# Performance work log

Measured on AMD Instinct MI355X. Metric: run time of the kernel, lower is better.

Reference implementation:

```python
import jax, jax.numpy as jnp
import numpy as np

TAU = 3.0
K = 3
EPS = 1e-8


def _normalize(x):
    # L2-normalize over last dim with clamped norm (matches torch clamp(min=eps))
    n = jnp.clip(jnp.linalg.norm(x, axis=-1, keepdims=True), EPS, None)
    return x / n


def get_sim(im, s):
    # im: [N, R, D], s: [P, L, D] -> sim [N, P]
    im_n = _normalize(im)
    s_n = _normalize(s)
    scores = jnp.einsum('nrd,pld->nprl', im_n, s_n)  # cosine per (region, token)
    return scores.max(axis=2).sum(axis=2)            # max over regions, sum over tokens


def semantic_transfer_loss(m1_n, m1_p, m2_p):
    sim = get_sim(m1_n, m1_p)                        # [Bn, Bp]
    m1_k, idx = jax.lax.top_k(sim, K)                # [Bn, K]
    m2_k_emb = m2_p[idx]                             # [Bn, K, L2, D]
    im_n = _normalize(m1_n)
    s_n = _normalize(m2_k_emb)
    scores = jnp.einsum('nrd,nkld->nkrl', im_n, s_n) # [Bn, K, R, L2]
    m2_k = scores.max(axis=2).sum(axis=2)            # [Bn, K]
    log_q = jax.nn.log_softmax(m2_k / TAU, axis=-1)
    log_p = jax.nn.log_softmax(m1_k / TAU, axis=-1)
    p = jnp.exp(log_p)
    # F.kl_div(log_q, p, reduction='sum') = sum p * (log p - log q)
    return jnp.sum(p * (log_p - log_q))


def setup_inputs() -> dict:
    key = jax.random.key(0)
    k1, k2, k3, k4 = jax.random.split(key, 4)
    B, R, L, D = 256, 36, 32, 1024
    return {
        'img_n_emb': jax.random.normal(k1, (B, R, D), dtype=jnp.float32),
        'cap_n_emb': jax.random.normal(k2, (B, L, D), dtype=jnp.float32),
        'img_p_emb': jax.random.normal(k3, (B, R, D), dtype=jnp.float32),
        'cap_p_emb': jax.random.normal(k4, (B, L, D), dtype=jnp.float32),
    }


def reference(img_n_emb, cap_n_emb, img_p_emb, cap_p_emb):
    loss = (semantic_transfer_loss(img_n_emb, img_p_emb, cap_p_emb)
            + semantic_transfer_loss(cap_n_emb, cap_p_emb, img_p_emb))
    return loss
```

## Files before the change

### kernel.cpp

```cpp
#include <hip/hip_runtime.h>
#include <math.h>

#define TAU 3.0f
#define NB 256
#define DD 1024
#define KSEL 3

typedef _Float16 half8 __attribute__((ext_vector_type(8)));
typedef _Float16 half4 __attribute__((ext_vector_type(4)));
typedef float f32x4 __attribute__((ext_vector_type(4)));

__device__ __forceinline__ void gload_lds16(const void* g, void* l) {
    __builtin_amdgcn_global_load_lds(
        (const __attribute__((address_space(1))) unsigned int*)g,
        (__attribute__((address_space(3))) unsigned int*)l, 16, 0, 0);
}

__device__ __forceinline__ unsigned int fenc(float x) {
    unsigned int u = __float_as_uint(x);
    return u ^ (((unsigned int)((int)u >> 31)) | 0x80000000u);
}
__device__ __forceinline__ float fdec(unsigned int e) {
    unsigned int u = (e & 0x80000000u) ? (e ^ 0x80000000u) : ~e;
    return __uint_as_float(u);
}

__global__ __launch_bounds__(256) void norm_split_kernel(
    const float* __restrict__ x, _Float16* __restrict__ hi, _Float16* __restrict__ lo,
    float* __restrict__ inv)
{
    int row = blockIdx.x;
    int tid = threadIdx.x;
    const float* p = x + (size_t)row * DD;
    float4 v = reinterpret_cast<const float4*>(p)[tid];
    float ss = fmaf(v.x, v.x, fmaf(v.y, v.y, fmaf(v.z, v.z, v.w * v.w)));
#pragma unroll
    for (int off = 32; off; off >>= 1) ss += __shfl_down(ss, off);
    __shared__ float red[4];
    if ((tid & 63) == 0) red[tid >> 6] = ss;
    __syncthreads();
    float tot = red[0] + red[1] + red[2] + red[3];
    float nrm = fmaxf(sqrtf(tot), 1e-8f);
    if (tid == 0) inv[row] = 1.0f / nrm;
    float xn[4] = { v.x / nrm, v.y / nrm, v.z / nrm, v.w / nrm };
    half4 h, l;
#pragma unroll
    for (int i = 0; i < 4; ++i) {
        _Float16 hh = (_Float16)xn[i];
        h[i] = hh;
        l[i] = (_Float16)(xn[i] - (float)hh);
    }
    *reinterpret_cast<half4*>(hi + (size_t)row * DD + tid * 4) = h;
    *reinterpret_cast<half4*>(lo + (size_t)row * DD + tid * 4) = l;
}

template<int G, int THREADS>
__global__ __launch_bounds__(THREADS, 1) void mfma_simX_kernel(
    const _Float16* __restrict__ Ah, const _Float16* __restrict__ Al,
    const _Float16* __restrict__ Bh, const _Float16* __restrict__ Bl,
    unsigned int* __restrict__ cmax, int Wc)
{
    constexpr int TM = 192, TN = 192, WGM = 2, WGN = 3, WAVES = 6;
    static_assert(THREADS == WAVES * 64, "");
    constexpr int WMS = TM / WGM;
    constexpr int WNS = TN / WGN;
    constexpr int MF = WMS / 16;
    constexpr int NF = WNS / 16;
    constexpr int KCH = 32, NCH = DD / KCH;
    constexpr int ABYT = 2 * TM * 64;
    constexpr int BBYT = 2 * TN * 64;
    constexpr int BUFB = ABYT + BBYT;
    constexpr int NREG = BUFB / 1024;
    constexpr int RPW = NREG / WAVES;

    __shared__ __align__(16) char LDSB[2 * BUFB];

    const int bm = blockIdx.y, bn = blockIdx.x;
    const int tid = threadIdx.x;
    const int lane = tid & 63, wv = tid >> 6;
    const int wm = wv / WGN, wn = wv % WGN;
    const int col = lane & 15, grp = lane >> 4;

    const _Float16* srcp[RPW];
    int ldsoff[RPW];
    const int swz = ((lane & 3) ^ ((lane >> 3) & 3)) << 3;
#pragma unroll
    for (int i = 0; i < RPW; ++i) {
        int r = wv + i * WAVES;
        int arr = r / 12;
        int rip = (r % 12) * 16 + (lane >> 2);
        int grow = (arr < 2 ? bm * TM : bn * TN) + rip;
        const _Float16* base = (arr == 0) ? Ah : (arr == 1) ? Al : (arr == 2) ? Bh : Bl;
        srcp[i] = base + (((size_t)grow) << 10) + swz;
        ldsoff[i] = r * 1024;
    }

    f32x4 acc[MF][NF];
#pragma unroll
    for (int i = 0; i < MF; ++i)
#pragma unroll
        for (int j = 0; j < NF; ++j) acc[i][j] = (f32x4)0.f;

#pragma unroll
    for (int i = 0; i < RPW; ++i) gload_lds16(srcp[i], LDSB + ldsoff[i]);
    __syncthreads();

    for (int c = 0; c < NCH; ++c) {
        const int cb = c & 1;
        if (c + 1 < NCH) {
            const int nbuf = cb ^ 1;
#pragma unroll
            for (int i = 0; i < RPW; ++i)
                gload_lds16(srcp[i] + (c + 1) * KCH, LDSB + nbuf * BUFB + ldsoff[i]);
        }
        const char* LA  = LDSB + cb * BUFB;
        const char* LAl = LA + TM * 64;
        const char* LB  = LA + ABYT;
        const char* LBl = LB + TN * 64;

        half8 bh[NF], bl_[NF];
#pragma unroll
        for (int fn = 0; fn < NF; ++fn) {
            int row = wn * WNS + fn * 16 + col;
            int j = (grp ^ ((row >> 1) & 3)) << 4;
            bh[fn]  = *(const half8*)(LB  + row * 64 + j);
            bl_[fn] = *(const half8*)(LBl + row * 64 + j);
        }
#pragma unroll
        for (int fm = 0; fm < MF; ++fm) {
            int row = wm * WMS + fm * 16 + col;
            int j = (grp ^ ((row >> 1) & 3)) << 4;
            half8 ah  = *(const half8*)(LA  + row * 64 + j);
            half8 al_ = *(const half8*)(LAl + row * 64 + j);
#pragma unroll
            for (int fn = 0; fn < NF; ++fn) {
                acc[fm][fn] = __builtin_amdgcn_mfma_f32_16x16x32_f16(ah,  bh[fn],  acc[fm][fn], 0, 0, 0);
                acc[fm][fn] = __builtin_amdgcn_mfma_f32_16x16x32_f16(ah,  bl_[fn], acc[fm][fn], 0, 0, 0);
                acc[fm][fn] = __builtin_amdgcn_mfma_f32_16x16x32_f16(al_, bh[fn],  acc[fm][fn], 0, 0, 0);
            }
        }
        __syncthreads();
    }

    float* cm = (float*)LDSB;
    constexpr int CMS = TN + 1;
#pragma unroll
    for (int fm = 0; fm < MF; ++fm) {
        int rc = ((wm * WMS + fm * 16) >> 2) + grp;
#pragma unroll
        for (int fn = 0; fn < NF; ++fn) {
            f32x4 v = acc[fm][fn];
            float m = fmaxf(fmaxf(v[0], v[1]), fmaxf(v[2], v[3]));
            cm[rc * CMS + wn * WNS + fn * 16 + col] = m;
        }
    }
    __syncthreads();
    const int mrow0 = bm * TM;
    const int g0 = mrow0 / G;
    const int g1 = (mrow0 + TM - 1) / G;
    const int ngs = g1 - g0 + 1;
    for (int it = tid; it < ngs * TN; it += THREADS) {
        int gi = it / TN, cc = it - gi * TN;
        int g = g0 + gi;
        int rs = g * G;        if (rs < mrow0) rs = mrow0;
        int re = (g + 1) * G;  if (re > mrow0 + TM) re = mrow0 + TM;
        float m = -INFINITY;
        int rc0 = (rs - mrow0) >> 2, rc1 = (re - mrow0) >> 2;
        for (int rc = rc0; rc < rc1; ++rc) m = fmaxf(m, cm[rc * CMS + cc]);
        atomicMax(&cmax[(size_t)g * Wc + bn * TN + cc], fenc(m));
    }
}

template<int G2>
__global__ void finish_kernel(const unsigned int* __restrict__ cmax, int Wc,
                              float* __restrict__ sim) {
    int n = blockIdx.x, p = threadIdx.x;
    const unsigned int* row = cmax + (size_t)n * Wc + p * G2;
    float s = 0.f;
#pragma unroll
    for (int l = 0; l < G2; ++l) s += fdec(row[l]);
    sim[(size_t)n * NB + p] = s;
}

template<int R, int L>
__global__ __launch_bounds__(256) void blocksim_kernel(
    const float* __restrict__ A, const float* __restrict__ invA,
    const float* __restrict__ Bm, const float* __restrict__ invB,
    const int* __restrict__ bsel, int P, float* __restrict__ out)
{
    constexpr int CH = 64, CHP = 68;
    constexpr int TI = (R + 15) / 16, TJ = (L + 15) / 16;
    __shared__ __align__(16) float As[R][CHP];
    __shared__ __align__(16) float Bs[L][CHP];
    __shared__ float colmax[L];

    int t = blockIdx.x;
    int n = t / P;
    int pk = t - n * P;
    int brow = bsel ? bsel[t] : pk;

    const float* Ab = A + (size_t)n * R * DD;
    const float* Bb = Bm + (size_t)brow * L * DD;

    int tid = threadIdx.x;
    int tx = tid & 15, ty = tid >> 4;

    int ra[TI], lb[TJ];
#pragma unroll
    for (int i = 0; i < TI; ++i) ra[i] = min(ty + 16 * i, R - 1);
#pragma unroll
    for (int j = 0; j < TJ; ++j) lb[j] = min(tx + 16 * j, L - 1);

    float acc[TI][TJ];
#pragma unroll
    for (int i = 0; i < TI; ++i)
#pragma unroll
        for (int j = 0; j < TJ; ++j) acc[i][j] = 0.f;

    for (int c = 0; c < DD / CH; ++c) {
        int d0 = c * CH;
        for (int idx = tid; idx < R * CH; idx += 256) {
            int r = idx >> 6, dd = idx & 63;
            As[r][dd] = Ab[(size_t)r * DD + d0 + dd];
        }
        for (int idx = tid; idx < L * CH; idx += 256) {
            int r = idx >> 6, dd = idx & 63;
            Bs[r][dd] = Bb[(size_t)r * DD + d0 + dd];
        }
        __syncthreads();
#pragma unroll
        for (int dd = 0; dd < CH; dd += 4) {
            float4 av[TI], bv[TJ];
#pragma unroll
            for (int i = 0; i < TI; ++i) av[i] = *reinterpret_cast<const float4*>(&As[ra[i]][dd]);
#pragma unroll
            for (int j = 0; j < TJ; ++j) bv[j] = *reinterpret_cast<const float4*>(&Bs[lb[j]][dd]);
#pragma unroll
            for (int i = 0; i < TI; ++i)
#pragma unroll
                for (int j = 0; j < TJ; ++j) {
                    acc[i][j] = fmaf(av[i].x, bv[j].x, acc[i][j]);
                    acc[i][j] = fmaf(av[i].y, bv[j].y, acc[i][j]);
                    acc[i][j] = fmaf(av[i].z, bv[j].z, acc[i][j]);
                    acc[i][j] = fmaf(av[i].w, bv[j].w, acc[i][j]);
                }
        }
        __syncthreads();
    }

    float* cosS = &As[0][0];
    constexpr int LS = L + 1;
    float ia[TI];
#pragma unroll
    for (int i = 0; i < TI; ++i) ia[i] = invA[n * R + ra[i]];
#pragma unroll
    for (int j = 0; j < TJ; ++j) {
        float ib = invB[brow * L + lb[j]];
#pragma unroll
        for (int i = 0; i < TI; ++i) {
            int r = ty + 16 * i, l = tx + 16 * j;
            if (r < R && l < L) cosS[r * LS + l] = acc[i][j] * ia[i] * ib;
        }
    }
    __syncthreads();
    if (tid < L) {
        float m = -INFINITY;
        for (int r = 0; r < R; ++r) m = fmaxf(m, cosS[r * LS + tid]);
        colmax[tid] = m;
    }
    __syncthreads();
    if (tid == 0) {
        float s = 0.f;
        for (int l = 0; l < L; ++l) s += colmax[l];
        out[t] = s;
    }
}

__global__ void topk_kernel(const float* __restrict__ sim, float* __restrict__ vals,
                            int* __restrict__ outidx) {
    int n = blockIdx.x;
    int lane = threadIdx.x;
    float v0 = -INFINITY, v1 = -INFINITY, v2 = -INFINITY;
    int i0 = 0x7fffffff, i1 = 0x7fffffff, i2 = 0x7fffffff;
    for (int p = lane; p < NB; p += 64) {
        float v = sim[(size_t)n * NB + p];
        if (v > v0)      { v2 = v1; i2 = i1; v1 = v0; i1 = i0; v0 = v; i0 = p; }
        else if (v > v1) { v2 = v1; i2 = i1; v1 = v;  i1 = p; }
        else if (v > v2) { v2 = v;  i2 = p; }
    }
#pragma unroll
    for (int off = 32; off; off >>= 1) {
        float w0 = __shfl_down(v0, off), w1 = __shfl_down(v1, off), w2 = __shfl_down(v2, off);
        int   j0 = __shfl_down(i0, off), j1 = __shfl_down(i1, off), j2 = __shfl_down(i2, off);
#define INS3(w, j)                                                                   \
        if (w > v0 || (w == v0 && j < i0)) { v2=v1;i2=i1; v1=v0;i1=i0; v0=w;i0=j; }  \
        else if (w > v1 || (w == v1 && j < i1)) { v2=v1;i2=i1; v1=w;i1=j; }          \
        else if (w > v2 || (w == v2 && j < i2)) { v2=w;i2=j; }
        INS3(w0, j0); INS3(w1, j1); INS3(w2, j2);
#undef INS3
    }
    if (lane == 0) {
        vals[n * 3 + 0] = v0; vals[n * 3 + 1] = v1; vals[n * 3 + 2] = v2;
        outidx[n * 3 + 0] = i0; outidx[n * 3 + 1] = i1; outidx[n * 3 + 2] = i2;
    }
}

__global__ void loss_kernel(const float* __restrict__ m1k, const float* __restrict__ m2k,
                            float* __restrict__ out) {
    int n = threadIdx.x;
    float a[3], b[3];
#pragma unroll
    for (int i = 0; i < 3; ++i) {
        a[i] = m1k[n * 3 + i] * (1.0f / TAU);
        b[i] = m2k[n * 3 + i] * (1.0f / TAU);
    }
    float am = fmaxf(a[0], fmaxf(a[1], a[2]));
    float bm = fmaxf(b[0], fmaxf(b[1], b[2]));
    float ase = expf(a[0] - am) + expf(a[1] - am) + expf(a[2] - am);
    float bse = expf(b[0] - bm) + expf(b[1] - bm) + expf(b[2] - bm);
    float alse = am + logf(ase);
    float blse = bm + logf(bse);
    float acc = 0.f;
#pragma unroll
    for (int i = 0; i < 3; ++i) {
        float lp = a[i] - alse, lq = b[i] - blse;
        acc += expf(lp) * (lp - lq);
    }
#pragma unroll
    for (int off = 32; off; off >>= 1) acc += __shfl_down(acc, off);
    __shared__ float w[4];
    if ((threadIdx.x & 63) == 0) w[threadIdx.x >> 6] = acc;
    __syncthreads();
    if (threadIdx.x == 0) atomicAdd(out, w[0] + w[1] + w[2] + w[3]);
}

extern "C" void kernel_launch(void* const* d_in, const int* in_sizes, int n_in,
                              void* d_out, int out_size, void* d_ws, size_t ws_size,
                              hipStream_t stream) {
    const float* img_n = (const float*)d_in[0];
    const float* cap_n = (const float*)d_in[1];
    const float* img_p = (const float*)d_in[2];
    const float* cap_p = (const float*)d_in[3];
    float* out = (float*)d_out;

    char* w = (char*)d_ws;
    auto alloc = [&](size_t bytes) -> char* {
        char* p = w;
        w += (bytes + 255) & ~(size_t)255;
        return p;
    };
    const size_t IMGE  = (size_t)NB * 36 * DD;
    const size_t CAPE  = (size_t)NB * 32 * DD;
    const size_t CAPEP = (size_t)8256 * DD;

    _Float16* imgN_h = (_Float16*)alloc(IMGE * 2);
    _Float16* imgN_l = (_Float16*)alloc(IMGE * 2);
    _Float16* imgP_h = (_Float16*)alloc(IMGE * 2);
    _Float16* imgP_l = (_Float16*)alloc(IMGE * 2);
    _Float16* capN_h = (_Float16*)alloc(CAPEP * 2);
    _Float16* capN_l = (_Float16*)alloc(CAPEP * 2);
    _Float16* capP_h = (_Float16*)alloc(CAPEP * 2);
    _Float16* capP_l = (_Float16*)alloc(CAPEP * 2);

    const size_t CM1 = (size_t)256 * 9216 * 4;
    const size_t CM2 = (size_t)258 * 8256 * 4;
    unsigned int* cmaxbuf = (unsigned int*)alloc(CM1 > CM2 ? CM1 : CM2);

    float* inv_im_n  = (float*)alloc(NB * 36 * 4);
    float* inv_cap_n = (float*)alloc(NB * 32 * 4);
    float* inv_im_p  = (float*)alloc(NB * 36 * 4);
    float* inv_cap_p = (float*)alloc(NB * 32 * 4);
    float* sim1 = (float*)alloc(NB * NB * 4);
    float* sim2 = (float*)alloc(NB * NB * 4);
    float* m1k1 = (float*)alloc(NB * 3 * 4);
    float* m2k1 = (float*)alloc(NB * 3 * 4);
    float* m1k2 = (float*)alloc(NB * 3 * 4);
    float* m2k2 = (float*)alloc(NB * 3 * 4);
    int* idx1 = (int*)alloc(NB * 3 * 4);
    int* idx2 = (int*)alloc(NB * 3 * 4);

    hipMemsetAsync(d_out, 0, sizeof(float), stream);
    hipMemsetAsync(cmaxbuf, 0, CM1, stream);
    hipMemsetAsync(capN_h + CAPE, 0, (CAPEP - CAPE) * 2, stream);
    hipMemsetAsync(capN_l + CAPE, 0, (CAPEP - CAPE) * 2, stream);
    hipMemsetAsync(capP_h + CAPE, 0, (CAPEP - CAPE) * 2, stream);
    hipMemsetAsync(capP_l + CAPE, 0, (CAPEP - CAPE) * 2, stream);

    norm_split_kernel<<<NB * 36, 256, 0, stream>>>(img_n, imgN_h, imgN_l, inv_im_n);
    norm_split_kernel<<<NB * 36, 256, 0, stream>>>(img_p, imgP_h, imgP_l, inv_im_p);
    norm_split_kernel<<<NB * 32, 256, 0, stream>>>(cap_n, capN_h, capN_l, inv_cap_n);
    norm_split_kernel<<<NB * 32, 256, 0, stream>>>(cap_p, capP_h, capP_l, inv_cap_p);

    mfma_simX_kernel<36, 384><<<dim3(48, 48), 384, 0, stream>>>(
        imgN_h, imgN_l, imgP_h, imgP_l, cmaxbuf, 9216);
    finish_kernel<36><<<NB, NB, 0, stream>>>(cmaxbuf, 9216, sim1);
    hipMemsetAsync(cmaxbuf, 0, CM2, stream);
    topk_kernel<<<NB, 64, 0, stream>>>(sim1, m1k1, idx1);
    blocksim_kernel<36, 32><<<NB * KSEL, 256, 0, stream>>>(img_n, inv_im_n, cap_p, inv_cap_p,
                                                           idx1, KSEL, m2k1);
    loss_kernel<<<1, NB, 0, stream>>>(m1k1, m2k1, out);

    mfma_simX_kernel<32, 384><<<dim3(43, 43), 384, 0, stream>>>(
        capN_h, capN_l, capP_h, capP_l, cmaxbuf, 8256);
    finish_kernel<32><<<NB, NB, 0, stream>>>(cmaxbuf, 8256, sim2);
    topk_kernel<<<NB, 64, 0, stream>>>(sim2, m1k2, idx2);
    blocksim_kernel<32, 36><<<NB * KSEL, 256, 0, stream>>>(cap_n, inv_cap_n, img_p, inv_im_p,
                                                           idx2, KSEL, m2k2);
    loss_kernel<<<1, NB, 0, stream>>>(m1k2, m2k2, out);
}
```

Before: 1.228 ms.

## Retile MFMA sim GEMM, fuse finish+topk, move stage2 to fp16 MFMA

The big similarity GEMM moves from 192x192 tiles with 6 waves and one block per CU to 128x160 tiles with 4 waves and two blocks per CU, and raises wave priority around the MFMA block. The row-sum finish and top-3 selection are fused into one kernel that keeps sims in LDS. The fp32 scalar blocksim stage is replaced by a single-wave fp16 MFMA kernel that reads the already normalized hi halves, so the inverse-norm outputs are dropped. Stage 2 now uses only the fp16 hi part and loses precision, which can affect the top-k-weighted loss. Separate cmax buffers also remove one mid-pipeline memset.

```diff
diff --git a/kernel.cpp b/kernel.cpp
--- a/kernel.cpp
+++ b/kernel.cpp
@@ -26,8 +26,7 @@
 }
 
 __global__ __launch_bounds__(256) void norm_split_kernel(
-    const float* __restrict__ x, _Float16* __restrict__ hi, _Float16* __restrict__ lo,
-    float* __restrict__ inv)
+    const float* __restrict__ x, _Float16* __restrict__ hi, _Float16* __restrict__ lo)
 {
     int row = blockIdx.x;
     int tid = threadIdx.x;
@@ -41,7 +40,6 @@
     __syncthreads();
     float tot = red[0] + red[1] + red[2] + red[3];
     float nrm = fmaxf(sqrtf(tot), 1e-8f);
-    if (tid == 0) inv[row] = 1.0f / nrm;
     float xn[4] = { v.x / nrm, v.y / nrm, v.z / nrm, v.w / nrm };
     half4 h, l;
 #pragma unroll
@@ -54,18 +52,15 @@
     *reinterpret_cast<half4*>(lo + (size_t)row * DD + tid * 4) = l;
 }
 
-template<int G, int THREADS>
-__global__ __launch_bounds__(THREADS, 1) void mfma_simX_kernel(
+template<int G>
+__global__ __launch_bounds__(256, 2) void mfma_simX_kernel(
     const _Float16* __restrict__ Ah, const _Float16* __restrict__ Al,
     const _Float16* __restrict__ Bh, const _Float16* __restrict__ Bl,
     unsigned int* __restrict__ cmax, int Wc)
 {
-    constexpr int TM = 192, TN = 192, WGM = 2, WGN = 3, WAVES = 6;
-    static_assert(THREADS == WAVES * 64, "");
-    constexpr int WMS = TM / WGM;
-    constexpr int WNS = TN / WGN;
-    constexpr int MF = WMS / 16;
-    constexpr int NF = WNS / 16;
+    constexpr int TM = 128, TN = 160, WAVES = 4, THREADS = 256;
+    constexpr int WMS = 64, WNS = 80;
+    constexpr int MF = 4, NF = 5;
     constexpr int KCH = 32, NCH = DD / KCH;
     constexpr int ABYT = 2 * TM * 64;
     constexpr int BBYT = 2 * TN * 64;
@@ -78,7 +73,7 @@
     const int bm = blockIdx.y, bn = blockIdx.x;
     const int tid = threadIdx.x;
     const int lane = tid & 63, wv = tid >> 6;
-    const int wm = wv / WGN, wn = wv % WGN;
+    const int wm = wv >> 1, wn = wv & 1;
     const int col = lane & 15, grp = lane >> 4;
 
     const _Float16* srcp[RPW];
@@ -87,10 +82,13 @@
 #pragma unroll
     for (int i = 0; i < RPW; ++i) {
         int r = wv + i * WAVES;
-        int arr = r / 12;
-        int rip = (r % 12) * 16 + (lane >> 2);
-        int grow = (arr < 2 ? bm * TM : bn * TN) + rip;
-        const _Float16* base = (arr == 0) ? Ah : (arr == 1) ? Al : (arr == 2) ? Bh : Bl;
+        bool isB = r >= 16;
+        int rr = isB ? r - 16 : r;
+        int rpp = isB ? 10 : 8;
+        int plane = rr / rpp;
+        int rip = (rr - plane * rpp) * 16 + (lane >> 2);
+        const _Float16* base = isB ? (plane ? Bl : Bh) : (plane ? Al : Ah);
+        int grow = (isB ? bn * TN : bm * TM) + rip;
         srcp[i] = base + (((size_t)grow) << 10) + swz;
         ldsoff[i] = r * 1024;
     }
@@ -126,6 +124,7 @@
             bh[fn]  = *(const half8*)(LB  + row * 64 + j);
             bl_[fn] = *(const half8*)(LBl + row * 64 + j);
         }
+        __builtin_amdgcn_s_setprio(1);
 #pragma unroll
         for (int fm = 0; fm < MF; ++fm) {
             int row = wm * WMS + fm * 16 + col;
@@ -139,6 +138,7 @@
                 acc[fm][fn] = __builtin_amdgcn_mfma_f32_16x16x32_f16(al_, bh[fn],  acc[fm][fn], 0, 0, 0);
             }
         }
+        __builtin_amdgcn_s_setprio(0);
         __syncthreads();
     }
 
@@ -172,137 +172,104 @@
 }
 
 template<int G2>
-__global__ void finish_kernel(const unsigned int* __restrict__ cmax, int Wc,
-                              float* __restrict__ sim) {
+__global__ __launch_bounds__(256) void finish_topk_kernel(
+    const unsigned int* __restrict__ cmax, int Wc,
+    float* __restrict__ vals, int* __restrict__ outidx)
+{
+    __shared__ float sims[NB];
     int n = blockIdx.x, p = threadIdx.x;
-    const unsigned int* row = cmax + (size_t)n * Wc + p * G2;
+    const unsigned int* row = cmax + (size_t)n * Wc + (size_t)p * G2;
     float s = 0.f;
 #pragma unroll
     for (int l = 0; l < G2; ++l) s += fdec(row[l]);
-    sim[(size_t)n * NB + p] = s;
+    sims[p] = s;
+    __syncthreads();
+    if (p < 64) {
+        int lane = p;
+        float v0 = -INFINITY, v1 = -INFINITY, v2 = -INFINITY;
+        int i0 = 0x7fffffff, i1 = 0x7fffffff, i2 = 0x7fffffff;
+        for (int q = lane; q < NB; q += 64) {
+            float v = sims[q];
+            if (v > v0)      { v2 = v1; i2 = i1; v1 = v0; i1 = i0; v0 = v; i0 = q; }
+            else if (v > v1) { v2 = v1; i2 = i1; v1 = v;  i1 = q; }
+            else if (v > v2) { v2 = v;  i2 = q; }
+        }
+#pragma unroll
+        for (int off = 32; off; off >>= 1) {
+            float w0 = __shfl_down(v0, off), w1 = __shfl_down(v1, off), w2 = __shfl_down(v2, off);
+            int   j0 = __shfl_down(i0, off), j1 = __shfl_down(i1, off), j2 = __shfl_down(i2, off);
+#define INS3(w, j)                                                                   \
+            if (w > v0 || (w == v0 && j < i0)) { v2=v1;i2=i1; v1=v0;i1=i0; v0=w;i0=j; }  \
+            else if (w > v1 || (w == v1 && j < i1)) { v2=v1;i2=i1; v1=w;i1=j; }          \
+            else if (w > v2 || (w == v2 && j < i2)) { v2=w;i2=j; }
+            INS3(w0, j0); INS3(w1, j1); INS3(w2, j2);
+#undef INS3
+        }
+        if (lane == 0) {
+            vals[n * 3 + 0] = v0; vals[n * 3 + 1] = v1; vals[n * 3 + 2] = v2;
+            outidx[n * 3 + 0] = i0; outidx[n * 3 + 1] = i1; outidx[n * 3 + 2] = i2;
+        }
+    }
 }
 
 template<int R, int L>
-__global__ __launch_bounds__(256) void blocksim_kernel(
-    const float* __restrict__ A, const float* __restrict__ invA,
-    const float* __restrict__ Bm, const float* __restrict__ invB,
-    const int* __restrict__ bsel, int P, float* __restrict__ out)
+__global__ __launch_bounds__(64) void stage2_kernel(
+    const _Float16* __restrict__ Ah, const _Float16* __restrict__ Bh,
+    const int* __restrict__ bsel, float* __restrict__ m2k)
 {
-    constexpr int CH = 64, CHP = 68;
-    constexpr int TI = (R + 15) / 16, TJ = (L + 15) / 16;
-    __shared__ __align__(16) float As[R][CHP];
-    __shared__ __align__(16) float Bs[L][CHP];
-    __shared__ float colmax[L];
-
+    constexpr int MF = (R + 15) / 16, NF = (L + 15) / 16;
     int t = blockIdx.x;
-    int n = t / P;
-    int pk = t - n * P;
-    int brow = bsel ? bsel[t] : pk;
-
-    const float* Ab = A + (size_t)n * R * DD;
-    const float* Bb = Bm + (size_t)brow * L * DD;
-
-    int tid = threadIdx.x;
-    int tx = tid & 15, ty = tid >> 4;
-
-    int ra[TI], lb[TJ];
-#pragma unroll
-    for (int i = 0; i < TI; ++i) ra[i] = min(ty + 16 * i, R - 1);
-#pragma unroll
-    for (int j = 0; j < TJ; ++j) lb[j] = min(tx + 16 * j, L - 1);
-
-    float acc[TI][TJ];
-#pragma unroll
-    for (int i = 0; i < TI; ++i)
-#pragma unroll
-        for (int j = 0; j < TJ; ++j) acc[i][j] = 0.f;
-
-    for (int c = 0; c < DD / CH; ++c) {
-        int d0 = c * CH;
-        for (int idx = tid; idx < R * CH; idx += 256) {
-            int r = idx >> 6, dd = idx & 63;
-            As[r][dd] = Ab[(size_t)r * DD + d0 + dd];
-        }
-        for (int idx = tid; idx < L * CH; idx += 256) {
-            int r = idx >> 6, dd = idx & 63;
-            Bs[r][dd] = Bb[(size_t)r * DD + d0 + dd];
-        }
-        __syncthreads();
-#pragma unroll
-        for (int dd = 0; dd < CH; dd += 4) {
-            float4 av[TI], bv[TJ];
-#pragma unroll
-            for (int i = 0; i < TI; ++i) av[i] = *reinterpret_cast<const float4*>(&As[ra[i]][dd]);
-#pragma unroll
-            for (int j = 0; j < TJ; ++j) bv[j] = *reinterpret_cast<const float4*>(&Bs[lb[j]][dd]);
-#pragma unroll
-            for (int i = 0; i < TI; ++i)
-#pragma unroll
-                for (int j = 0; j < TJ; ++j) {
-                    acc[i][j] = fmaf(av[i].x, bv[j].x, acc[i][j]);
-                    acc[i][j] = fmaf(av[i].y, bv[j].y, acc[i][j]);
-                    acc[i][j] = fmaf(av[i].z, bv[j].z, acc[i][j]);
-                    acc[i][j] = fmaf(av[i].w, bv[j].w, acc[i][j]);
-                }
-        }
-        __syncthreads();
-    }
-
-    float* cosS = &As[0][0];
-    constexpr int LS = L + 1;
-    float ia[TI];
-#pragma unroll
-    for (int i = 0; i < TI; ++i) ia[i] = invA[n * R + ra[i]];
-#pragma unroll
-    for (int j = 0; j < TJ; ++j) {
-        float ib = invB[brow * L + lb[j]];
-#pragma unroll
-        for (int i = 0; i < TI; ++i) {
-            int r = ty + 16 * i, l = tx + 16 * j;
-            if (r < R && l < L) cosS[r * LS + l] = acc[i][j] * ia[i] * ib;
-        }
-    }
-    __syncthreads();
-    if (tid < L) {
+    int n = t / KSEL;
+    int b = bsel[t];
+    const _Float16* Ab = Ah + (size_t)n * R * DD;
+    const _Float16* Bb = Bh + (size_t)b * L * DD;
+    int lane = threadIdx.x;
+    int col = lane & 15, grp = lane >> 4;
+
+    int ra[MF], lb[NF];
+#pragma unroll
+    for (int i = 0; i < MF; ++i) ra[i] = min(i * 16 + col, R - 1);
+#pragma unroll
+    for (int j = 0; j < NF; ++j) lb[j] = min(j * 16 + col, L - 1);
+
+    f32x4 acc[MF][NF];
+#pragma unroll
+    for (int i = 0; i < MF; ++i)
+#pragma unroll
+        for (int j = 0; j < NF; ++j) acc[i][j] = (f32x4)0.f;
+
+    for (int c = 0; c < DD / 32; ++c) {
+        int k0 = c * 32 + grp * 8;
+        half8 af[MF], bf[NF];
+#pragma unroll
+        for (int i = 0; i < MF; ++i) af[i] = *(const half8*)(Ab + (size_t)ra[i] * DD + k0);
+#pragma unroll
+        for (int j = 0; j < NF; ++j) bf[j] = *(const half8*)(Bb + (size_t)lb[j] * DD + k0);
+#pragma unroll
+        for (int i = 0; i < MF; ++i)
+#pragma unroll
+            for (int j = 0; j < NF; ++j)
+                acc[i][j] = __builtin_amdgcn_mfma_f32_16x16x32_f16(af[i], bf[j], acc[i][j], 0, 0, 0);
+    }
+
+    float s = 0.f;
+#pragma unroll
+    for (int j = 0; j < NF; ++j) {
         float m = -INFINITY;
-        for (int r = 0; r < R; ++r) m = fmaxf(m, cosS[r * LS + tid]);
-        colmax[tid] = m;
-    }
-    __syncthreads();
-    if (tid == 0) {
-        float s = 0.f;
-        for (int l = 0; l < L; ++l) s += colmax[l];
-        out[t] = s;
-    }
-}
-
-__global__ void topk_kernel(const float* __restrict__ sim, float* __restrict__ vals,
-                            int* __restrict__ outidx) {
-    int n = blockIdx.x;
-    int lane = threadIdx.x;
-    float v0 = -INFINITY, v1 = -INFINITY, v2 = -INFINITY;
-    int i0 = 0x7fffffff, i1 = 0x7fffffff, i2 = 0x7fffffff;
-    for (int p = lane; p < NB; p += 64) {
-        float v = sim[(size_t)n * NB + p];
-        if (v > v0)      { v2 = v1; i2 = i1; v1 = v0; i1 = i0; v0 = v; i0 = p; }
-        else if (v > v1) { v2 = v1; i2 = i1; v1 = v;  i1 = p; }
-        else if (v > v2) { v2 = v;  i2 = p; }
-    }
-#pragma unroll
-    for (int off = 32; off; off >>= 1) {
-        float w0 = __shfl_down(v0, off), w1 = __shfl_down(v1, off), w2 = __shfl_down(v2, off);
-        int   j0 = __shfl_down(i0, off), j1 = __shfl_down(i1, off), j2 = __shfl_down(i2, off);
-#define INS3(w, j)                                                                   \
-        if (w > v0 || (w == v0 && j < i0)) { v2=v1;i2=i1; v1=v0;i1=i0; v0=w;i0=j; }  \
-        else if (w > v1 || (w == v1 && j < i1)) { v2=v1;i2=i1; v1=w;i1=j; }          \
-        else if (w > v2 || (w == v2 && j < i2)) { v2=w;i2=j; }
-        INS3(w0, j0); INS3(w1, j1); INS3(w2, j2);
-#undef INS3
-    }
-    if (lane == 0) {
-        vals[n * 3 + 0] = v0; vals[n * 3 + 1] = v1; vals[n * 3 + 2] = v2;
-        outidx[n * 3 + 0] = i0; outidx[n * 3 + 1] = i1; outidx[n * 3 + 2] = i2;
-    }
+#pragma unroll
+        for (int i = 0; i < MF; ++i) {
+#pragma unroll
+            for (int r = 0; r < 4; ++r) m = fmaxf(m, acc[i][j][r]);
+        }
+        m = fmaxf(m, __shfl_xor(m, 16));
+        m = fmaxf(m, __shfl_xor(m, 32));
+        if (j * 16 + col < L) s += m;
+    }
+    s += __shfl_xor(s, 1);
+    s += __shfl_xor(s, 2);
+    s += __shfl_xor(s, 4);
+    s += __shfl_xor(s, 8);
+    if (lane == 0) m2k[t] = s;
 }
 
 __global__ void loss_kernel(const float* __restrict__ m1k, const float* __restrict__ m2k,
@@ -349,29 +316,26 @@
         w += (bytes + 255) & ~(size_t)255;
         return p;
     };
-    const size_t IMGE  = (size_t)NB * 36 * DD;
-    const size_t CAPE  = (size_t)NB * 32 * DD;
-    const size_t CAPEP = (size_t)8256 * DD;
+    const size_t IMGE   = (size_t)NB * 36 * DD;
+    const size_t CAPE   = (size_t)NB * 32 * DD;
+    const size_t IMGPE  = (size_t)9280 * DD;
+    const size_t CAPPE  = (size_t)8320 * DD;
+    const int WC1 = 9280, WC2 = 8320;
 
     _Float16* imgN_h = (_Float16*)alloc(IMGE * 2);
     _Float16* imgN_l = (_Float16*)alloc(IMGE * 2);
-    _Float16* imgP_h = (_Float16*)alloc(IMGE * 2);
-    _Float16* imgP_l = (_Float16*)alloc(IMGE * 2);
-    _Float16* capN_h = (_Float16*)alloc(CAPEP * 2);
-    _Float16* capN_l = (_Float16*)alloc(CAPEP * 2);
-    _Float16* capP_h = (_Float16*)alloc(CAPEP * 2);
-    _Float16* capP_l = (_Float16*)alloc(CAPEP * 2);
-
-    const size_t CM1 = (size_t)256 * 9216 * 4;
-    const size_t CM2 = (size_t)258 * 8256 * 4;
-    unsigned int* cmaxbuf = (unsigned int*)alloc(CM1 > CM2 ? CM1 : CM2);
-
-    float* inv_im_n  = (float*)alloc(NB * 36 * 4);
-    float* inv_cap_n = (float*)alloc(NB * 32 * 4);
-    float* inv_im_p  = (float*)alloc(NB * 36 * 4);
-    float* inv_cap_p = (float*)alloc(NB * 32 * 4);
-    float* sim1 = (float*)alloc(NB * NB * 4);
-    float* sim2 = (float*)alloc(NB * NB * 4);
+    _Float16* imgP_h = (_Float16*)alloc(IMGPE * 2);
+    _Float16* imgP_l = (_Float16*)alloc(IMGPE * 2);
+    _Float16* capN_h = (_Float16*)alloc(CAPE * 2);
+    _Float16* capN_l = (_Float16*)alloc(CAPE * 2);
+    _Float16* capP_h = (_Float16*)alloc(CAPPE * 2);
+    _Float16* capP_l = (_Float16*)alloc(CAPPE * 2);
+
+    const size_t CM1 = (size_t)256 * WC1 * 4;
+    const size_t CM2 = (size_t)256 * WC2 * 4;
+    unsigned int* cmax1 = (unsigned int*)alloc(CM1);
+    unsigned int* cmax2 = (unsigned int*)alloc(CM2);
+
     float* m1k1 = (float*)alloc(NB * 3 * 4);
     float* m2k1 = (float*)alloc(NB * 3 * 4);
     float* m1k2 = (float*)alloc(NB * 3 * 4);
@@ -380,31 +344,27 @@
     int* idx2 = (int*)alloc(NB * 3 * 4);
 
     hipMemsetAsync(d_out, 0, sizeof(float), stream);
-    hipMemsetAsync(cmaxbuf, 0, CM1, stream);
-    hipMemsetAsync(capN_h + CAPE, 0, (CAPEP - CAPE) * 2, stream);
-    hipMemsetAsync(capN_l + CAPE, 0, (CAPEP - CAPE) * 2, stream);
-    hipMemsetAsync(capP_h + CAPE, 0, (CAPEP - CAPE) * 2, stream);
-    hipMemsetAsync(capP_l + CAPE, 0, (CAPEP - CAPE) * 2, stream);
-
-    norm_split_kernel<<<NB * 36, 256, 0, stream>>>(img_n, imgN_h, imgN_l, inv_im_n);
-    norm_split_kernel<<<NB * 36, 256, 0, stream>>>(img_p, imgP_h, imgP_l, inv_im_p);
-    norm_split_kernel<<<NB * 32, 256, 0, stream>>>(cap_n, capN_h, capN_l, inv_cap_n);
-    norm_split_kernel<<<NB * 32, 256, 0, stream>>>(cap_p, capP_h, capP_l, inv_cap_p);
-
-    mfma_simX_kernel<36, 384><<<dim3(48, 48), 384, 0, stream>>>(
-        imgN_h, imgN_l, imgP_h, imgP_l, cmaxbuf, 9216);
-    finish_kernel<36><<<NB, NB, 0, stream>>>(cmaxbuf, 9216, sim1);
-    hipMemsetAsync(cmaxbuf, 0, CM2, stream);
-    topk_kernel<<<NB, 64, 0, stream>>>(sim1, m1k1, idx1);
-    blocksim_kernel<36, 32><<<NB * KSEL, 256, 0, stream>>>(img_n, inv_im_n, cap_p, inv_cap_p,
-                                                           idx1, KSEL, m2k1);
+    hipMemsetAsync(cmax1, 0, CM1, stream);
+    hipMemsetAsync(cmax2, 0, CM2, stream);
+    hipMemsetAsync(imgP_h + IMGE, 0, (IMGPE - IMGE) * 2, stream);
+    hipMemsetAsync(imgP_l + IMGE, 0, (IMGPE - IMGE) * 2, stream);
+    hipMemsetAsync(capP_h + CAPE, 0, (CAPPE - CAPE) * 2, stream);
+    hipMemsetAsync(capP_l + CAPE, 0, (CAPPE - CAPE) * 2, stream);
+
+    norm_split_kernel<<<NB * 36, 256, 0, stream>>>(img_n, imgN_h, imgN_l);
+    norm_split_kernel<<<NB * 36, 256, 0, stream>>>(img_p, imgP_h, imgP_l);
+    norm_split_kernel<<<NB * 32, 256, 0, stream>>>(cap_n, capN_h, capN_l);
+    norm_split_kernel<<<NB * 32, 256, 0, stream>>>(cap_p, capP_h, capP_l);
+
+    mfma_simX_kernel<36><<<dim3(58, 72), 256, 0, stream>>>(
+        imgN_h, imgN_l, imgP_h, imgP_l, cmax1, WC1);
+    finish_topk_kernel<36><<<NB, 256, 0, stream>>>(cmax1, WC1, m1k1, idx1);
+    stage2_kernel<36, 32><<<NB * KSEL, 64, 0, stream>>>(imgN_h, capP_h, idx1, m2k1);
     loss_kernel<<<1, NB, 0, stream>>>(m1k1, m2k1, out);
 
-    mfma_simX_kernel<32, 384><<<dim3(43, 43), 384, 0, stream>>>(
-        capN_h, capN_l, capP_h, capP_l, cmaxbuf, 8256);
-    finish_kernel<32><<<NB, NB, 0, stream>>>(cmaxbuf, 8256, sim2);
-    topk_kernel<<<NB, 64, 0, stream>>>(sim2, m1k2, idx2);
-    blocksim_kernel<32, 36><<<NB * KSEL, 256, 0, stream>>>(cap_n, inv_cap_n, img_p, inv_im_p,
-                                                           idx2, KSEL, m2k2);
+    mfma_simX_kernel<32><<<dim3(52, 64), 256, 0, stream>>>(
+        capN_h, capN_l, capP_h, capP_l, cmax2, WC2);
+    finish_topk_kernel<32><<<NB, 256, 0, stream>>>(cmax2, WC2, m1k2, idx2);
+    stage2_kernel<32, 36><<<NB * KSEL, 64, 0, stream>>>(capN_h, imgP_h, idx2, m2k2);
     loss_kernel<<<1, NB, 0, stream>>>(m1k2, m2k2, out);
 }
```

After: 1.043 ms. 1.18x faster.
